# Performance work log

Measured on AMD Instinct MI355X. Metric: run time of the kernel, lower is better.

## Reference

```python
import jax, jax.numpy as jnp
import numpy as np
from jax import lax

B, T, I, H, O = 256, 512, 64, 128, 2  # batch, seq_len, input_size, hidden_size, output_size


def gru_layer(x, Wih, Whh, bih, bhh, reverse):
    # x: [B,T,in_dim], Wih: [3H,in_dim], Whh: [3H,H]; PyTorch gate order: r, z, n
    xw = jnp.einsum('bti,gi->btg', x, Wih) + bih  # precompute input projections [B,T,3H]

    def step(h, xw_t):
        gh = h @ Whh.T + bhh  # [B,3H]
        r = jax.nn.sigmoid(xw_t[:, :H] + gh[:, :H])
        z = jax.nn.sigmoid(xw_t[:, H:2 * H] + gh[:, H:2 * H])
        n = jnp.tanh(xw_t[:, 2 * H:] + r * gh[:, 2 * H:])
        h_new = (1.0 - z) * n + z * h
        return h_new, h_new

    h0 = jnp.zeros((x.shape[0], H), x.dtype)
    _, hs = lax.scan(step, h0, jnp.swapaxes(xw, 0, 1), reverse=reverse)
    # lax.scan with reverse=True stacks outputs aligned to original time order,
    # matching PyTorch's bidirectional GRU output layout.
    return jnp.swapaxes(hs, 0, 1)  # [B,T,H]


def gru_forward(x, params, fc_w, fc_b):
    h = x
    for (Wf, Uf, bf, cf, Wb, Ub, bb, cb) in params:
        fwd = gru_layer(h, Wf, Uf, bf, cf, reverse=False)
        bwd = gru_layer(h, Wb, Ub, bb, cb, reverse=True)
        h = jnp.concatenate([fwd, bwd], axis=-1)  # [B,T,2H]
    last = jax.nn.relu(h[:, -1, :])  # relu then take last timestep (equivalent order)
    return last @ fc_w.T + fc_b  # [B,O]


def setup_inputs() -> dict:
    key = jax.random.key(0)
    ks = iter(jax.random.split(key, 24))
    s = 1.0 / np.sqrt(H)  # PyTorch GRU init scale
    u = lambda shape: jax.random.uniform(next(ks), shape, jnp.float32, -s, s)
    inp = {"x": jax.random.normal(next(ks), (B, T, I), jnp.float32)}
    for l, in_dim in enumerate([I, 2 * H]):
        for d in ("f", "b"):
            inp[f"Wih{l}{d}"] = u((3 * H, in_dim))
            inp[f"Whh{l}{d}"] = u((3 * H, H))
            inp[f"bih{l}{d}"] = u((3 * H,))
            inp[f"bhh{l}{d}"] = u((3 * H,))
    inp["fc_w"] = u((O, 2 * H))
    inp["fc_b"] = u((O,))
    return inp


def reference(x, Wih0f, Whh0f, bih0f, bhh0f, Wih0b, Whh0b, bih0b, bhh0b,
              Wih1f, Whh1f, bih1f, bhh1f, Wih1b, Whh1b, bih1b, bhh1b,
              fc_w, fc_b):
    params = [(Wih0f, Whh0f, bih0f, bhh0f, Wih0b, Whh0b, bih0b, bhh0b),
              (Wih1f, Whh1f, bih1f, bhh1f, Wih1b, Whh1b, bih1b, bhh1b)]
    return gru_forward(x, params, fc_w, fc_b)
```

## Files before the change

kernel.cpp:

```cpp
#include <hip/hip_runtime.h>
#include <hip/hip_fp16.h>

#define B_  256
#define T_  512
#define I_  64
#define H_  128
#define G_  384
#define HC  256

#define O_OUT0 0ull
#define O_XW1  67108864ull
#define O_X16  O_XW1
#define O_WP   167772160ull
#define O_H1F  (O_WP + 196608ull)
#define O_WF16 (O_H1F + 131072ull)

typedef _Float16 h8 __attribute__((ext_vector_type(8)));
typedef _Float16 h2 __attribute__((ext_vector_type(2)));
typedef float    f4 __attribute__((ext_vector_type(4)));

#define MFMA16 __builtin_amdgcn_mfma_f32_16x16x32_f16

__device__ __forceinline__ float sigm(float x)   { return __builtin_amdgcn_rcpf(1.f + __expf(-x)); }
__device__ __forceinline__ float tanh_f(float x) { return 1.f - 2.f * __builtin_amdgcn_rcpf(1.f + __expf(2.f * x)); }

__device__ __forceinline__ void bar_lds() {
    asm volatile("s_waitcnt lgkmcnt(0)\n\ts_barrier" ::: "memory");
}

__device__ __forceinline__ h8 load_w8(const float* src) {
    f4 a = *(const f4*)src;
    f4 b = *(const f4*)(src + 4);
    h8 v;
    v[0]=(_Float16)a[0]; v[1]=(_Float16)a[1]; v[2]=(_Float16)a[2]; v[3]=(_Float16)a[3];
    v[4]=(_Float16)b[0]; v[5]=(_Float16)b[1]; v[6]=(_Float16)b[2]; v[7]=(_Float16)b[3];
    return v;
}

__global__ void prep(const float* __restrict__ x, _Float16* __restrict__ x16,
                     const float* __restrict__ Wf, _Float16* __restrict__ wf16,
                     const float* __restrict__ W1b, __half2* __restrict__ wp) {
    const int bid = blockIdx.x;
    const int tid = threadIdx.x;
    if (bid < 4096) {
        int i = bid * 256 + tid;
        const float* s = x + (size_t)i * 8;
        f4 a = *(const f4*)s, b = *(const f4*)(s + 4);
        h8 v;
        v[0]=(_Float16)a[0]; v[1]=(_Float16)a[1]; v[2]=(_Float16)a[2]; v[3]=(_Float16)a[3];
        v[4]=(_Float16)b[0]; v[5]=(_Float16)b[1]; v[6]=(_Float16)b[2]; v[7]=(_Float16)b[3];
        *(h8*)(x16 + (size_t)i * 8) = v;
    } else if (bid < 4144) {
        int i = (bid - 4096) * 256 + tid;
        const float* s = Wf + (size_t)i * 8;
        f4 a = *(const f4*)s, b = *(const f4*)(s + 4);
        h8 v;
        v[0]=(_Float16)a[0]; v[1]=(_Float16)a[1]; v[2]=(_Float16)a[2]; v[3]=(_Float16)a[3];
        v[4]=(_Float16)b[0]; v[5]=(_Float16)b[1]; v[6]=(_Float16)b[2]; v[7]=(_Float16)b[3];
        *(h8*)(wf16 + (size_t)i * 8) = v;
    } else {
        int i = (bid - 4144) * 256 + tid;
        int c = i % G_;
        int k2 = i / G_;
        wp[i] = __halves2half2(__float2half(W1b[c * 256 + 2 * k2]),
                               __float2half(W1b[c * 256 + 2 * k2 + 1]));
    }
}

__launch_bounds__(512, 1)
__global__ void scan_l0(const _Float16* __restrict__ x16,
                        const float* __restrict__ Wih_f, const float* __restrict__ Whh_f,
                        const float* __restrict__ bih_f, const float* __restrict__ bhh_f,
                        const float* __restrict__ Wih_b, const float* __restrict__ Whh_b,
                        const float* __restrict__ bih_b, const float* __restrict__ bhh_b,
                        _Float16* __restrict__ out0) {
    __shared__ __align__(16) _Float16 s_h[2][16 * 128];

    const int tid  = threadIdx.x;
    const int lane = tid & 63;
    const int w    = tid >> 6;
    const int dir  = blockIdx.y;
    const int b0   = blockIdx.x * 4;

    const float* Wih = dir ? Wih_b : Wih_f;
    const float* Whh = dir ? Whh_b : Whh_f;
    const float* bih = dir ? bih_b : bih_f;
    const float* bhh = dir ? bhh_b : bhh_f;

    for (int i = tid; i < 2 * 16 * 128; i += 512) ((_Float16*)s_h)[i] = (_Float16)0.f;

    const int ln15 = lane & 15;
    const int lq   = lane >> 4;
    const int col  = 16 * w + ln15;

    h8 bh[3][4], bx[3][2];
    float seedR = bih[col] + bhh[col];
    float seedZ = bih[H_ + col] + bhh[H_ + col];
    float bihN  = bih[2 * H_ + col];
    float bhhN  = bhh[2 * H_ + col];
#pragma unroll
    for (int g = 0; g < 3; g++) {
        int n = g * H_ + col;
#pragma unroll
        for (int kt = 0; kt < 4; kt++) bh[g][kt] = load_w8(Whh + (size_t)n * H_ + kt * 32 + lq * 8);
#pragma unroll
        for (int kt = 0; kt < 2; kt++) bx[g][kt] = load_w8(Wih + (size_t)n * I_ + kt * 32 + lq * 8);
    }
    const int arow = ln15 & 12;
    int offh[4];
#pragma unroll
    for (int kt = 0; kt < 4; kt++)
        offh[kt] = arow * 128 + (((kt * 4 + lq) ^ arow) & 15) * 8;
    const int row0  = lq * 4;
    const int offw0 = row0 * 128 + ((((col >> 3) ^ row0) & 15)) * 8 + (col & 7);

    const _Float16* xbase = x16 + ((size_t)(b0 + (ln15 >> 2)) * T_) * I_ + lq * 8;

    const f4 z4 = (f4){0.f, 0.f, 0.f, 0.f};
    const f4 sR4 = (f4){seedR, seedR, seedR, seedR};
    const f4 sZ4 = (f4){seedZ, seedZ, seedZ, seedZ};
    const f4 sXn4 = (f4){bihN, bihN, bihN, bihN};
    const f4 sHn4 = (f4){bhhN, bhhN, bhhN, bhhN};

    _Float16* op = out0 + ((size_t)(b0 + lq) * T_ + (dir ? (T_ - 1) : 0)) * HC + dir * H_ + col;
    const int ostep = dir ? -HC : HC;
    const _Float16* xpA = xbase + (size_t)(dir ? (T_ - 4) : 3) * I_;
    const _Float16* xpB = xbase + (size_t)(dir ? (T_ - 5) : 4) * I_;
    const int xstep = dir ? -(2 * I_) : (2 * I_);

    float hF = 0.f;
    float xr0, xz0, xn0, xr1, xz1, xn1;
    h8 xvA0, xvA1, xvB0, xvB1;
    {
        int t0 = dir ? (T_ - 1) : 0;
        int t1 = dir ? (T_ - 2) : 1;
        int t2 = dir ? (T_ - 3) : 2;
        h8 xc0 = *(const h8*)(xbase + (size_t)t0 * I_);
        h8 xc1 = *(const h8*)(xbase + (size_t)t0 * I_ + 32);
        xvA0 = *(const h8*)(xbase + (size_t)t1 * I_);
        xvA1 = *(const h8*)(xbase + (size_t)t1 * I_ + 32);
        xvB0 = *(const h8*)(xbase + (size_t)t2 * I_);
        xvB1 = *(const h8*)(xbase + (size_t)t2 * I_ + 32);
        f4 aXr = MFMA16(xc1, bx[0][1], MFMA16(xc0, bx[0][0], sR4, 0, 0, 0), 0, 0, 0);
        f4 aXz = MFMA16(xc1, bx[1][1], MFMA16(xc0, bx[1][0], sZ4, 0, 0, 0), 0, 0, 0);
        f4 aXn = MFMA16(xc1, bx[2][1], MFMA16(xc0, bx[2][0], sXn4, 0, 0, 0), 0, 0, 0);
        xr0 = aXr[0]; xz0 = aXz[0]; xn0 = aXn[0];
    }
    __syncthreads();

#pragma unroll 1
    for (int t = 0; t < T_; t += 2) {
        {
            h8 ah0 = *(const h8*)&s_h[0][offh[0]];
            h8 ah1 = *(const h8*)&s_h[0][offh[1]];
            h8 ah2 = *(const h8*)&s_h[0][offh[2]];
            h8 ah3 = *(const h8*)&s_h[0][offh[3]];
            f4 hRa = MFMA16(ah1, bh[0][1], MFMA16(ah0, bh[0][0], z4, 0, 0, 0), 0, 0, 0);
            f4 hRb = MFMA16(ah3, bh[0][3], MFMA16(ah2, bh[0][2], z4, 0, 0, 0), 0, 0, 0);
            f4 hZa = MFMA16(ah1, bh[1][1], MFMA16(ah0, bh[1][0], z4, 0, 0, 0), 0, 0, 0);
            f4 hZb = MFMA16(ah3, bh[1][3], MFMA16(ah2, bh[1][2], z4, 0, 0, 0), 0, 0, 0);
            f4 hNa = MFMA16(ah1, bh[2][1], MFMA16(ah0, bh[2][0], sHn4, 0, 0, 0), 0, 0, 0);
            f4 hNb = MFMA16(ah3, bh[2][3], MFMA16(ah2, bh[2][2], z4, 0, 0, 0), 0, 0, 0);
            float r = sigm(xr0 + hRa[0] + hRb[0]);
            float z = sigm(xz0 + hZa[0] + hZb[0]);
            float n = tanh_f(xn0 + r * (hNa[0] + hNb[0]));
            float h = n + z * (hF - n);
            hF = h;
            s_h[1][offw0] = (_Float16)h;
            *op = (_Float16)h; op += ostep;
            {
                f4 aXr = MFMA16(xvA1, bx[0][1], MFMA16(xvA0, bx[0][0], sR4, 0, 0, 0), 0, 0, 0);
                f4 aXz = MFMA16(xvA1, bx[1][1], MFMA16(xvA0, bx[1][0], sZ4, 0, 0, 0), 0, 0, 0);
                f4 aXn = MFMA16(xvA1, bx[2][1], MFMA16(xvA0, bx[2][0], sXn4, 0, 0, 0), 0, 0, 0);
                xr1 = aXr[0]; xz1 = aXz[0]; xn1 = aXn[0];
            }
            if (t + 3 < T_) {
                xvA0 = *(const h8*)(xpA);
                xvA1 = *(const h8*)(xpA + 32);
                xpA += xstep;
            }
            bar_lds();
        }
        {
            h8 ah0 = *(const h8*)&s_h[1][offh[0]];
            h8 ah1 = *(const h8*)&s_h[1][offh[1]];
            h8 ah2 = *(const h8*)&s_h[1][offh[2]];
            h8 ah3 = *(const h8*)&s_h[1][offh[3]];
            f4 hRa = MFMA16(ah1, bh[0][1], MFMA16(ah0, bh[0][0], z4, 0, 0, 0), 0, 0, 0);
            f4 hRb = MFMA16(ah3, bh[0][3], MFMA16(ah2, bh[0][2], z4, 0, 0, 0), 0, 0, 0);
            f4 hZa = MFMA16(ah1, bh[1][1], MFMA16(ah0, bh[1][0], z4, 0, 0, 0), 0, 0, 0);
            f4 hZb = MFMA16(ah3, bh[1][3], MFMA16(ah2, bh[1][2], z4, 0, 0, 0), 0, 0, 0);
            f4 hNa = MFMA16(ah1, bh[2][1], MFMA16(ah0, bh[2][0], sHn4, 0, 0, 0), 0, 0, 0);
            f4 hNb = MFMA16(ah3, bh[2][3], MFMA16(ah2, bh[2][2], z4, 0, 0, 0), 0, 0, 0);
            float r = sigm(xr1 + hRa[0] + hRb[0]);
            float z = sigm(xz1 + hZa[0] + hZb[0]);
            float n = tanh_f(xn1 + r * (hNa[0] + hNb[0]));
            float h = n + z * (hF - n);
            hF = h;
            s_h[0][offw0] = (_Float16)h;
            *op = (_Float16)h; op += ostep;
            if (t + 2 < T_) {
                f4 aXr = MFMA16(xvB1, bx[0][1], MFMA16(xvB0, bx[0][0], sR4, 0, 0, 0), 0, 0, 0);
                f4 aXz = MFMA16(xvB1, bx[1][1], MFMA16(xvB0, bx[1][0], sZ4, 0, 0, 0), 0, 0, 0);
                f4 aXn = MFMA16(xvB1, bx[2][1], MFMA16(xvB0, bx[2][0], sXn4, 0, 0, 0), 0, 0, 0);
                xr0 = aXr[0]; xz0 = aXz[0]; xn0 = aXn[0];
            }
            if (t + 4 < T_) {
                xvB0 = *(const h8*)(xpB);
                xvB1 = *(const h8*)(xpB + 32);
                xpB += xstep;
            }
            bar_lds();
        }
    }
}

__launch_bounds__(256, 1)
__global__ void gemm_xw1(const _Float16* __restrict__ A,
                         const _Float16* __restrict__ Bw,
                         const float* __restrict__ bias,
                         _Float16* __restrict__ C) {
    __shared__ __align__(16) _Float16 sA[2][64 * 64];
    __shared__ __align__(16) _Float16 sB[2][384 * 64];
    const int tid  = threadIdx.x;
    const int lane = tid & 63;
    const int w    = tid >> 6;
    const int wm   = w & 1, wn = w >> 1;
    const int ln15 = lane & 15, lq = lane >> 4;
    const size_t m0 = (size_t)blockIdx.x * 64;

    f4 acc[2][12] = {};

    int aRow[2], aG[2], aOff[2];
#pragma unroll
    for (int k = 0; k < 2; k++) {
        int idx = k * 256 + tid;
        aRow[k] = idx >> 3; aG[k] = idx & 7;
        aOff[k] = aRow[k] * 64 + ((aG[k] ^ (aRow[k] & 7)) & 7) * 8;
    }
    int bRow[12], bG[12], bOff[12];
#pragma unroll
    for (int k = 0; k < 12; k++) {
        int idx = k * 256 + tid;
        bRow[k] = idx >> 3; bG[k] = idx & 7;
        bOff[k] = bRow[k] * 64 + ((bG[k] ^ (bRow[k] & 7)) & 7) * 8;
    }
    int offA[2][2], offB[12][2];
#pragma unroll
    for (int mt = 0; mt < 2; mt++)
#pragma unroll
        for (int kt = 0; kt < 2; kt++) {
            int row = wm * 32 + mt * 16 + ln15;
            offA[mt][kt] = row * 64 + (((kt * 4 + lq) ^ (row & 7)) & 7) * 8;
        }
#pragma unroll
    for (int nt = 0; nt < 12; nt++)
#pragma unroll
        for (int kt = 0; kt < 2; kt++) {
            int row = wn * 192 + nt * 16 + ln15;
            offB[nt][kt] = row * 64 + (((kt * 4 + lq) ^ (row & 7)) & 7) * 8;
        }

    {
        h8 av[2], bv[12];
#pragma unroll
        for (int k = 0; k < 2; k++) av[k] = *(const h8*)(A + (m0 + aRow[k]) * 256 + aG[k] * 8);
#pragma unroll
        for (int k = 0; k < 12; k++) bv[k] = *(const h8*)(Bw + (size_t)bRow[k] * 256 + bG[k] * 8);
#pragma unroll
        for (int k = 0; k < 2; k++) *(h8*)&sA[0][aOff[k]] = av[k];
#pragma unroll
        for (int k = 0; k < 12; k++) *(h8*)&sB[0][bOff[k]] = bv[k];
        bar_lds();
    }

#pragma unroll
    for (int c = 0; c < 4; c++) {
        const int cur = c & 1;
        h8 av[2], bv[12];
        if (c < 3) {
#pragma unroll
            for (int k = 0; k < 2; k++)
                av[k] = *(const h8*)(A + (m0 + aRow[k]) * 256 + (c + 1) * 64 + aG[k] * 8);
#pragma unroll
            for (int k = 0; k < 12; k++)
                bv[k] = *(const h8*)(Bw + (size_t)bRow[k] * 256 + (c + 1) * 64 + bG[k] * 8);
        }
#pragma unroll
        for (int kt = 0; kt < 2; kt++) {
            h8 af0 = *(const h8*)&sA[cur][offA[0][kt]];
            h8 af1 = *(const h8*)&sA[cur][offA[1][kt]];
#pragma unroll
            for (int nt = 0; nt < 12; nt++) {
                h8 bf = *(const h8*)&sB[cur][offB[nt][kt]];
                acc[0][nt] = MFMA16(af0, bf, acc[0][nt], 0, 0, 0);
                acc[1][nt] = MFMA16(af1, bf, acc[1][nt], 0, 0, 0);
            }
        }
        if (c < 3) {
#pragma unroll
            for (int k = 0; k < 2; k++) *(h8*)&sA[cur ^ 1][aOff[k]] = av[k];
#pragma unroll
            for (int k = 0; k < 12; k++) *(h8*)&sB[cur ^ 1][bOff[k]] = bv[k];
            bar_lds();
        }
    }
#pragma unroll
    for (int nt = 0; nt < 12; nt++) {
        int col = wn * 192 + nt * 16 + ln15;
        float bb = bias[col];
        int pcol = (col < 256) ? ((col & 127) * 2 + (col >> 7)) : col;
#pragma unroll
        for (int mt = 0; mt < 2; mt++) {
            size_t row = m0 + wm * 32 + mt * 16 + lq * 4;
#pragma unroll
            for (int reg = 0; reg < 4; reg++)
                C[(row + reg) * G_ + pcol] = (_Float16)(acc[mt][nt][reg] + bb);
        }
    }
}

__launch_bounds__(512, 1)
__global__ void scan_l1(const _Float16* __restrict__ xw1,
                        const float* __restrict__ Whh,
                        const float* __restrict__ bhh,
                        float* __restrict__ h1f) {
    __shared__ __align__(16) _Float16 s_h[2][16 * 128];

    const int tid  = threadIdx.x;
    const int lane = tid & 63;
    const int w    = tid >> 6;
    const int b0   = blockIdx.x * 4;

    for (int i = tid; i < 2 * 16 * 128; i += 512) ((_Float16*)s_h)[i] = (_Float16)0.f;

    const int ln15 = lane & 15;
    const int lq   = lane >> 4;
    const int col  = 16 * w + ln15;

    h8 bh[3][4];
    float bhhF[3];
#pragma unroll
    for (int g = 0; g < 3; g++) {
        int n = g * H_ + col;
        bhhF[g] = bhh[n];
#pragma unroll
        for (int kt = 0; kt < 4; kt++) bh[g][kt] = load_w8(Whh + (size_t)n * H_ + kt * 32 + lq * 8);
    }
    const int arow = ln15 & 12;
    int offh[4];
#pragma unroll
    for (int kt = 0; kt < 4; kt++)
        offh[kt] = arow * 128 + (((kt * 4 + lq) ^ arow) & 15) * 8;
    const int row0  = lq * 4;
    const int offw0 = row0 * 128 + ((((col >> 3) ^ row0) & 15)) * 8 + (col & 7);

    const _Float16* rzbase = xw1 + ((size_t)(b0 + lq) * T_) * G_ + 2 * col;
    const _Float16* nbase  = xw1 + ((size_t)(b0 + lq) * T_) * G_ + 256 + col;

    const f4 z4 = (f4){0.f, 0.f, 0.f, 0.f};
    const f4 sR4 = (f4){bhhF[0], bhhF[0], bhhF[0], bhhF[0]};
    const f4 sZ4 = (f4){bhhF[1], bhhF[1], bhhF[1], bhhF[1]};
    const f4 sN4 = (f4){bhhF[2], bhhF[2], bhhF[2], bhhF[2]};

    __syncthreads();

    float hF = 0.f;
    h2 rzA = *(const h2*)(rzbase);
    h2 rzB = *(const h2*)(rzbase + G_);
    _Float16 nA = *nbase;
    _Float16 nB = *(nbase + G_);
    const _Float16* rzP2 = rzbase + 2 * G_;
    const _Float16* nP2  = nbase  + 2 * G_;
    const _Float16* rzP3 = rzbase + 3 * G_;
    const _Float16* nP3  = nbase  + 3 * G_;

#pragma unroll 1
    for (int s = 0; s < T_; s += 2) {
        {
            h8 ah0 = *(const h8*)&s_h[0][offh[0]];
            h8 ah1 = *(const h8*)&s_h[0][offh[1]];
            h8 ah2 = *(const h8*)&s_h[0][offh[2]];
            h8 ah3 = *(const h8*)&s_h[0][offh[3]];
            float xr = (float)rzA[0], xz = (float)rzA[1], xn = (float)nA;
            if (s + 2 < T_) {
                rzA = *(const h2*)rzP2;
                nA  = *nP2;
                rzP2 += 2 * G_; nP2 += 2 * G_;
            }
            f4 hRa = MFMA16(ah1, bh[0][1], MFMA16(ah0, bh[0][0], sR4, 0, 0, 0), 0, 0, 0);
            f4 hRb = MFMA16(ah3, bh[0][3], MFMA16(ah2, bh[0][2], z4, 0, 0, 0), 0, 0, 0);
            f4 hZa = MFMA16(ah1, bh[1][1], MFMA16(ah0, bh[1][0], sZ4, 0, 0, 0), 0, 0, 0);
            f4 hZb = MFMA16(ah3, bh[1][3], MFMA16(ah2, bh[1][2], z4, 0, 0, 0), 0, 0, 0);
            f4 hNa = MFMA16(ah1, bh[2][1], MFMA16(ah0, bh[2][0], sN4, 0, 0, 0), 0, 0, 0);
            f4 hNb = MFMA16(ah3, bh[2][3], MFMA16(ah2, bh[2][2], z4, 0, 0, 0), 0, 0, 0);
            float r = sigm(xr + hRa[0] + hRb[0]);
            float z = sigm(xz + hZa[0] + hZb[0]);
            float n = tanh_f(xn + r * (hNa[0] + hNb[0]));
            float h = n + z * (hF - n);
            hF = h;
            s_h[1][offw0] = (_Float16)h;
            bar_lds();
        }
        {
            h8 ah0 = *(const h8*)&s_h[1][offh[0]];
            h8 ah1 = *(const h8*)&s_h[1][offh[1]];
            h8 ah2 = *(const h8*)&s_h[1][offh[2]];
            h8 ah3 = *(const h8*)&s_h[1][offh[3]];
            float xr = (float)rzB[0], xz = (float)rzB[1], xn = (float)nB;
            if (s + 3 < T_) {
                rzB = *(const h2*)rzP3;
                nB  = *nP3;
                rzP3 += 2 * G_; nP3 += 2 * G_;
            }
            f4 hRa = MFMA16(ah1, bh[0][1], MFMA16(ah0, bh[0][0], sR4, 0, 0, 0), 0, 0, 0);
            f4 hRb = MFMA16(ah3, bh[0][3], MFMA16(ah2, bh[0][2], z4, 0, 0, 0), 0, 0, 0);
            f4 hZa = MFMA16(ah1, bh[1][1], MFMA16(ah0, bh[1][0], sZ4, 0, 0, 0), 0, 0, 0);
            f4 hZb = MFMA16(ah3, bh[1][3], MFMA16(ah2, bh[1][2], z4, 0, 0, 0), 0, 0, 0);
            f4 hNa = MFMA16(ah1, bh[2][1], MFMA16(ah0, bh[2][0], sN4, 0, 0, 0), 0, 0, 0);
            f4 hNb = MFMA16(ah3, bh[2][3], MFMA16(ah2, bh[2][2], z4, 0, 0, 0), 0, 0, 0);
            float r = sigm(xr + hRa[0] + hRb[0]);
            float z = sigm(xz + hZa[0] + hZb[0]);
            float n = tanh_f(xn + r * (hNa[0] + hNb[0]));
            float h = n + z * (hF - n);
            hF = h;
            s_h[0][offw0] = (_Float16)h;
            bar_lds();
        }
    }
    h1f[(size_t)(b0 + lq) * H_ + col] = hF;
}

__launch_bounds__(384)
__global__ void final_k(const _Float16* __restrict__ out0,
                        const float* __restrict__ h1f,
                        const __half2* __restrict__ w1b,
                        const float* __restrict__ bih1b, const float* __restrict__ bhh1b,
                        const float* __restrict__ fcw, const float* __restrict__ fcb,
                        float* __restrict__ out) {
    __shared__ __align__(16) float s_x1[HC];
    __shared__ __align__(16) float s_xw[G_];
    __shared__ __align__(16) float s_hc[HC];
    __shared__ float s_red[8];
    const int tid = threadIdx.x;
    const int b = blockIdx.x;
    if (tid < HC)
        s_x1[tid] = (float)out0[((size_t)b * T_ + (T_ - 1)) * HC + tid];
    __syncthreads();
    {
        float acc0 = 0.f, acc1 = 0.f;
        const float2* xv = (const float2*)s_x1;
#pragma unroll 8
        for (int k2 = 0; k2 < 128; k2 += 2) {
            float2 w0 = __half22float2(w1b[k2 * G_ + tid]);
            float2 w1 = __half22float2(w1b[(k2 + 1) * G_ + tid]);
            float2 a0 = xv[k2], a1 = xv[k2 + 1];
            acc0 += a0.x * w0.x + a0.y * w0.y;
            acc1 += a1.x * w1.x + a1.y * w1.y;
        }
        s_xw[tid] = bih1b[tid] + acc0 + acc1;
    }
    __syncthreads();
    if (tid < H_) {
        int j = tid;
        float rg = sigm(s_xw[j] + bhh1b[j]);
        float zg = sigm(s_xw[H_ + j] + bhh1b[H_ + j]);
        float ng = tanh_f(s_xw[2 * H_ + j] + rg * bhh1b[2 * H_ + j]);
        float hb = (1.f - zg) * ng;
        s_hc[H_ + j] = fmaxf(hb, 0.f);
        s_hc[j] = fmaxf(h1f[(size_t)b * H_ + j], 0.f);
    }
    __syncthreads();
    if (tid < HC) {
        float hv = s_hc[tid];
        float p0 = hv * fcw[tid];
        float p1 = hv * fcw[HC + tid];
#pragma unroll
        for (int off = 32; off; off >>= 1) {
            p0 += __shfl_down(p0, off);
            p1 += __shfl_down(p1, off);
        }
        if ((tid & 63) == 0) { s_red[(tid >> 6) * 2] = p0; s_red[(tid >> 6) * 2 + 1] = p1; }
    }
    __syncthreads();
    if (tid == 0) {
        out[b * 2 + 0] = fcb[0] + s_red[0] + s_red[2] + s_red[4] + s_red[6];
        out[b * 2 + 1] = fcb[1] + s_red[1] + s_red[3] + s_red[5] + s_red[7];
    }
}

extern "C" void kernel_launch(void* const* d_in, const int* in_sizes, int n_in,
                              void* d_out, int out_size, void* d_ws, size_t ws_size,
                              hipStream_t stream) {
    (void)in_sizes; (void)n_in; (void)out_size; (void)ws_size;
    const float* x     = (const float*)d_in[0];
    const float* Wih0f = (const float*)d_in[1];
    const float* Whh0f = (const float*)d_in[2];
    const float* bih0f = (const float*)d_in[3];
    const float* bhh0f = (const float*)d_in[4];
    const float* Wih0b = (const float*)d_in[5];
    const float* Whh0b = (const float*)d_in[6];
    const float* bih0b = (const float*)d_in[7];
    const float* bhh0b = (const float*)d_in[8];
    const float* Wih1f = (const float*)d_in[9];
    const float* Whh1f = (const float*)d_in[10];
    const float* bih1f = (const float*)d_in[11];
    const float* bhh1f = (const float*)d_in[12];
    const float* Wih1b = (const float*)d_in[13];
    const float* bih1b = (const float*)d_in[15];
    const float* bhh1b = (const float*)d_in[16];
    const float* fcw   = (const float*)d_in[17];
    const float* fcb   = (const float*)d_in[18];

    char* ws = (char*)d_ws;
    _Float16* out0 = (_Float16*)(ws + O_OUT0);
    _Float16* xw1  = (_Float16*)(ws + O_XW1);
    _Float16* x16  = (_Float16*)(ws + O_X16);
    __half2*  wp   = (__half2*)(ws + O_WP);
    float*    h1f  = (float*)(ws + O_H1F);
    _Float16* wf16 = (_Float16*)(ws + O_WF16);
    float*    out  = (float*)d_out;

    prep<<<4336, 256, 0, stream>>>(x, x16, Wih1f, wf16, Wih1b, wp);

    scan_l0<<<dim3(64, 2), 512, 0, stream>>>(x16, Wih0f, Whh0f, bih0f, bhh0f,
                                             Wih0b, Whh0b, bih0b, bhh0b, out0);

    gemm_xw1<<<2048, 256, 0, stream>>>(out0, wf16, bih1f, xw1);

    scan_l1<<<64, 512, 0, stream>>>(xw1, Whh1f, bhh1f, h1f);

    final_k<<<256, 384, 0, stream>>>(out0, h1f, wp, bih1b, bhh1b, fcw, fcb, out);
}
```

Baseline: 578.8 us.

## Process two independent batch groups per block in GRU scan kernels

Each scan block now handles 8 batch rows as two independent 4-row groups, with separate LDS hidden-state buffers, halving the grid for both layer-0 and layer-1 scans. The two independent MFMA chains are interleaved so that one group's matrix products and activations can hide the latency of the other within each serial timestep. MFMA accumulation is also reordered to interleave gates. In exchange the per-step work per block doubles, register pressure rises, and only 64 or 32 blocks run on the device, leaving most CUs idle.

```diff
diff --git a/kernel.cpp b/kernel.cpp
--- a/kernel.cpp
+++ b/kernel.cpp
@@ -74,20 +74,20 @@
                         const float* __restrict__ Wih_b, const float* __restrict__ Whh_b,
                         const float* __restrict__ bih_b, const float* __restrict__ bhh_b,
                         _Float16* __restrict__ out0) {
-    __shared__ __align__(16) _Float16 s_h[2][16 * 128];
+    __shared__ __align__(16) _Float16 s_h[2][2][16 * 128];
 
     const int tid  = threadIdx.x;
     const int lane = tid & 63;
     const int w    = tid >> 6;
     const int dir  = blockIdx.y;
-    const int b0   = blockIdx.x * 4;
+    const int b0   = blockIdx.x * 8;
 
     const float* Wih = dir ? Wih_b : Wih_f;
     const float* Whh = dir ? Whh_b : Whh_f;
     const float* bih = dir ? bih_b : bih_f;
     const float* bhh = dir ? bhh_b : bhh_f;
 
-    for (int i = tid; i < 2 * 16 * 128; i += 512) ((_Float16*)s_h)[i] = (_Float16)0.f;
+    for (int i = tid; i < 2 * 2 * 16 * 128; i += 512) ((_Float16*)s_h)[i] = (_Float16)0.f;
 
     const int ln15 = lane & 15;
     const int lq   = lane >> 4;
@@ -114,101 +114,147 @@
     const int row0  = lq * 4;
     const int offw0 = row0 * 128 + ((((col >> 3) ^ row0) & 15)) * 8 + (col & 7);
 
-    const _Float16* xbase = x16 + ((size_t)(b0 + (ln15 >> 2)) * T_) * I_ + lq * 8;
-
     const f4 z4 = (f4){0.f, 0.f, 0.f, 0.f};
     const f4 sR4 = (f4){seedR, seedR, seedR, seedR};
     const f4 sZ4 = (f4){seedZ, seedZ, seedZ, seedZ};
     const f4 sXn4 = (f4){bihN, bihN, bihN, bihN};
     const f4 sHn4 = (f4){bhhN, bhhN, bhhN, bhhN};
 
-    _Float16* op = out0 + ((size_t)(b0 + lq) * T_ + (dir ? (T_ - 1) : 0)) * HC + dir * H_ + col;
+    const _Float16* xbase[2];
+    _Float16* op[2];
+    const _Float16* xpA[2];
+    const _Float16* xpB[2];
+#pragma unroll
+    for (int g = 0; g < 2; g++) {
+        int bg = b0 + g * 4;
+        xbase[g] = x16 + ((size_t)(bg + (ln15 >> 2)) * T_) * I_ + lq * 8;
+        op[g] = out0 + ((size_t)(bg + lq) * T_ + (dir ? (T_ - 1) : 0)) * HC + dir * H_ + col;
+        xpA[g] = xbase[g] + (size_t)(dir ? (T_ - 4) : 3) * I_;
+        xpB[g] = xbase[g] + (size_t)(dir ? (T_ - 5) : 4) * I_;
+    }
     const int ostep = dir ? -HC : HC;
-    const _Float16* xpA = xbase + (size_t)(dir ? (T_ - 4) : 3) * I_;
-    const _Float16* xpB = xbase + (size_t)(dir ? (T_ - 5) : 4) * I_;
     const int xstep = dir ? -(2 * I_) : (2 * I_);
 
-    float hF = 0.f;
-    float xr0, xz0, xn0, xr1, xz1, xn1;
-    h8 xvA0, xvA1, xvB0, xvB1;
-    {
+    float hF[2] = {0.f, 0.f};
+    float xr0[2], xz0[2], xn0[2], xr1[2], xz1[2], xn1[2];
+    h8 xvA0[2], xvA1[2], xvB0[2], xvB1[2];
+#pragma unroll
+    for (int g = 0; g < 2; g++) {
         int t0 = dir ? (T_ - 1) : 0;
         int t1 = dir ? (T_ - 2) : 1;
         int t2 = dir ? (T_ - 3) : 2;
-        h8 xc0 = *(const h8*)(xbase + (size_t)t0 * I_);
-        h8 xc1 = *(const h8*)(xbase + (size_t)t0 * I_ + 32);
-        xvA0 = *(const h8*)(xbase + (size_t)t1 * I_);
-        xvA1 = *(const h8*)(xbase + (size_t)t1 * I_ + 32);
-        xvB0 = *(const h8*)(xbase + (size_t)t2 * I_);
-        xvB1 = *(const h8*)(xbase + (size_t)t2 * I_ + 32);
-        f4 aXr = MFMA16(xc1, bx[0][1], MFMA16(xc0, bx[0][0], sR4, 0, 0, 0), 0, 0, 0);
-        f4 aXz = MFMA16(xc1, bx[1][1], MFMA16(xc0, bx[1][0], sZ4, 0, 0, 0), 0, 0, 0);
-        f4 aXn = MFMA16(xc1, bx[2][1], MFMA16(xc0, bx[2][0], sXn4, 0, 0, 0), 0, 0, 0);
-        xr0 = aXr[0]; xz0 = aXz[0]; xn0 = aXn[0];
+        h8 xc0 = *(const h8*)(xbase[g] + (size_t)t0 * I_);
+        h8 xc1 = *(const h8*)(xbase[g] + (size_t)t0 * I_ + 32);
+        xvA0[g] = *(const h8*)(xbase[g] + (size_t)t1 * I_);
+        xvA1[g] = *(const h8*)(xbase[g] + (size_t)t1 * I_ + 32);
+        xvB0[g] = *(const h8*)(xbase[g] + (size_t)t2 * I_);
+        xvB1[g] = *(const h8*)(xbase[g] + (size_t)t2 * I_ + 32);
+        f4 aXr = sR4, aXz = sZ4, aXn = sXn4;
+        aXr = MFMA16(xc0, bx[0][0], aXr, 0, 0, 0);
+        aXz = MFMA16(xc0, bx[1][0], aXz, 0, 0, 0);
+        aXn = MFMA16(xc0, bx[2][0], aXn, 0, 0, 0);
+        aXr = MFMA16(xc1, bx[0][1], aXr, 0, 0, 0);
+        aXz = MFMA16(xc1, bx[1][1], aXz, 0, 0, 0);
+        aXn = MFMA16(xc1, bx[2][1], aXn, 0, 0, 0);
+        xr0[g] = aXr[0]; xz0[g] = aXz[0]; xn0[g] = aXn[0];
     }
     __syncthreads();
 
 #pragma unroll 1
     for (int t = 0; t < T_; t += 2) {
         {
-            h8 ah0 = *(const h8*)&s_h[0][offh[0]];
-            h8 ah1 = *(const h8*)&s_h[0][offh[1]];
-            h8 ah2 = *(const h8*)&s_h[0][offh[2]];
-            h8 ah3 = *(const h8*)&s_h[0][offh[3]];
-            f4 hRa = MFMA16(ah1, bh[0][1], MFMA16(ah0, bh[0][0], z4, 0, 0, 0), 0, 0, 0);
-            f4 hRb = MFMA16(ah3, bh[0][3], MFMA16(ah2, bh[0][2], z4, 0, 0, 0), 0, 0, 0);
-            f4 hZa = MFMA16(ah1, bh[1][1], MFMA16(ah0, bh[1][0], z4, 0, 0, 0), 0, 0, 0);
-            f4 hZb = MFMA16(ah3, bh[1][3], MFMA16(ah2, bh[1][2], z4, 0, 0, 0), 0, 0, 0);
-            f4 hNa = MFMA16(ah1, bh[2][1], MFMA16(ah0, bh[2][0], sHn4, 0, 0, 0), 0, 0, 0);
-            f4 hNb = MFMA16(ah3, bh[2][3], MFMA16(ah2, bh[2][2], z4, 0, 0, 0), 0, 0, 0);
-            float r = sigm(xr0 + hRa[0] + hRb[0]);
-            float z = sigm(xz0 + hZa[0] + hZb[0]);
-            float n = tanh_f(xn0 + r * (hNa[0] + hNb[0]));
-            float h = n + z * (hF - n);
-            hF = h;
-            s_h[1][offw0] = (_Float16)h;
-            *op = (_Float16)h; op += ostep;
-            {
-                f4 aXr = MFMA16(xvA1, bx[0][1], MFMA16(xvA0, bx[0][0], sR4, 0, 0, 0), 0, 0, 0);
-                f4 aXz = MFMA16(xvA1, bx[1][1], MFMA16(xvA0, bx[1][0], sZ4, 0, 0, 0), 0, 0, 0);
-                f4 aXn = MFMA16(xvA1, bx[2][1], MFMA16(xvA0, bx[2][0], sXn4, 0, 0, 0), 0, 0, 0);
-                xr1 = aXr[0]; xz1 = aXz[0]; xn1 = aXn[0];
-            }
-            if (t + 3 < T_) {
-                xvA0 = *(const h8*)(xpA);
-                xvA1 = *(const h8*)(xpA + 32);
-                xpA += xstep;
+            h8 ah[2][4];
+            f4 hRa[2], hRb[2], hZa[2], hZb[2], hNa[2], hNb[2];
+#pragma unroll
+            for (int g = 0; g < 2; g++) {
+#pragma unroll
+                for (int kt = 0; kt < 4; kt++) ah[g][kt] = *(const h8*)&s_h[g][0][offh[kt]];
+                hRa[g] = z4; hRb[g] = z4; hZa[g] = z4; hZb[g] = z4; hNa[g] = sHn4; hNb[g] = z4;
+                hRa[g] = MFMA16(ah[g][0], bh[0][0], hRa[g], 0, 0, 0);
+                hZa[g] = MFMA16(ah[g][0], bh[1][0], hZa[g], 0, 0, 0);
+                hNa[g] = MFMA16(ah[g][0], bh[2][0], hNa[g], 0, 0, 0);
+                hRb[g] = MFMA16(ah[g][2], bh[0][2], hRb[g], 0, 0, 0);
+                hZb[g] = MFMA16(ah[g][2], bh[1][2], hZb[g], 0, 0, 0);
+                hNb[g] = MFMA16(ah[g][2], bh[2][2], hNb[g], 0, 0, 0);
+                hRa[g] = MFMA16(ah[g][1], bh[0][1], hRa[g], 0, 0, 0);
+                hZa[g] = MFMA16(ah[g][1], bh[1][1], hZa[g], 0, 0, 0);
+                hNa[g] = MFMA16(ah[g][1], bh[2][1], hNa[g], 0, 0, 0);
+                hRb[g] = MFMA16(ah[g][3], bh[0][3], hRb[g], 0, 0, 0);
+                hZb[g] = MFMA16(ah[g][3], bh[1][3], hZb[g], 0, 0, 0);
+                hNb[g] = MFMA16(ah[g][3], bh[2][3], hNb[g], 0, 0, 0);
+            }
+#pragma unroll
+            for (int g = 0; g < 2; g++) {
+                float r = sigm(xr0[g] + hRa[g][0] + hRb[g][0]);
+                float z = sigm(xz0[g] + hZa[g][0] + hZb[g][0]);
+                float n = tanh_f(xn0[g] + r * (hNa[g][0] + hNb[g][0]));
+                float h = n + z * (hF[g] - n);
+                hF[g] = h;
+                s_h[g][1][offw0] = (_Float16)h;
+                *op[g] = (_Float16)h; op[g] += ostep;
+                {
+                    f4 aXr = sR4, aXz = sZ4, aXn = sXn4;
+                    aXr = MFMA16(xvA0[g], bx[0][0], aXr, 0, 0, 0);
+                    aXz = MFMA16(xvA0[g], bx[1][0], aXz, 0, 0, 0);
+                    aXn = MFMA16(xvA0[g], bx[2][0], aXn, 0, 0, 0);
+                    aXr = MFMA16(xvA1[g], bx[0][1], aXr, 0, 0, 0);
+                    aXz = MFMA16(xvA1[g], bx[1][1], aXz, 0, 0, 0);
+                    aXn = MFMA16(xvA1[g], bx[2][1], aXn, 0, 0, 0);
+                    xr1[g] = aXr[0]; xz1[g] = aXz[0]; xn1[g] = aXn[0];
+                }
+                if (t + 3 < T_) {
+                    xvA0[g] = *(const h8*)(xpA[g]);
+                    xvA1[g] = *(const h8*)(xpA[g] + 32);
+                    xpA[g] += xstep;
+                }
             }
             bar_lds();
         }
         {
-            h8 ah0 = *(const h8*)&s_h[1][offh[0]];
-            h8 ah1 = *(const h8*)&s_h[1][offh[1]];
-            h8 ah2 = *(const h8*)&s_h[1][offh[2]];
-            h8 ah3 = *(const h8*)&s_h[1][offh[3]];
-            f4 hRa = MFMA16(ah1, bh[0][1], MFMA16(ah0, bh[0][0], z4, 0, 0, 0), 0, 0, 0);
-            f4 hRb = MFMA16(ah3, bh[0][3], MFMA16(ah2, bh[0][2], z4, 0, 0, 0), 0, 0, 0);
-            f4 hZa = MFMA16(ah1, bh[1][1], MFMA16(ah0, bh[1][0], z4, 0, 0, 0), 0, 0, 0);
-            f4 hZb = MFMA16(ah3, bh[1][3], MFMA16(ah2, bh[1][2], z4, 0, 0, 0), 0, 0, 0);
-            f4 hNa = MFMA16(ah1, bh[2][1], MFMA16(ah0, bh[2][0], sHn4, 0, 0, 0), 0, 0, 0);
-            f4 hNb = MFMA16(ah3, bh[2][3], MFMA16(ah2, bh[2][2], z4, 0, 0, 0), 0, 0, 0);
-            float r = sigm(xr1 + hRa[0] + hRb[0]);
-            float z = sigm(xz1 + hZa[0] + hZb[0]);
-            float n = tanh_f(xn1 + r * (hNa[0] + hNb[0]));
-            float h = n + z * (hF - n);
-            hF = h;
-            s_h[0][offw0] = (_Float16)h;
-            *op = (_Float16)h; op += ostep;
-            if (t + 2 < T_) {
-                f4 aXr = MFMA16(xvB1, bx[0][1], MFMA16(xvB0, bx[0][0], sR4, 0, 0, 0), 0, 0, 0);
-                f4 aXz = MFMA16(xvB1, bx[1][1], MFMA16(xvB0, bx[1][0], sZ4, 0, 0, 0), 0, 0, 0);
-                f4 aXn = MFMA16(xvB1, bx[2][1], MFMA16(xvB0, bx[2][0], sXn4, 0, 0, 0), 0, 0, 0);
-                xr0 = aXr[0]; xz0 = aXz[0]; xn0 = aXn[0];
-            }
-            if (t + 4 < T_) {
-                xvB0 = *(const h8*)(xpB);
-                xvB1 = *(const h8*)(xpB + 32);
-                xpB += xstep;
+            h8 ah[2][4];
+            f4 hRa[2], hRb[2], hZa[2], hZb[2], hNa[2], hNb[2];
+#pragma unroll
+            for (int g = 0; g < 2; g++) {
+#pragma unroll
+                for (int kt = 0; kt < 4; kt++) ah[g][kt] = *(const h8*)&s_h[g][1][offh[kt]];
+                hRa[g] = z4; hRb[g] = z4; hZa[g] = z4; hZb[g] = z4; hNa[g] = sHn4; hNb[g] = z4;
+                hRa[g] = MFMA16(ah[g][0], bh[0][0], hRa[g], 0, 0, 0);
+                hZa[g] = MFMA16(ah[g][0], bh[1][0], hZa[g], 0, 0, 0);
+                hNa[g] = MFMA16(ah[g][0], bh[2][0], hNa[g], 0, 0, 0);
+                hRb[g] = MFMA16(ah[g][2], bh[0][2], hRb[g], 0, 0, 0);
+                hZb[g] = MFMA16(ah[g][2], bh[1][2], hZb[g], 0, 0, 0);
+                hNb[g] = MFMA16(ah[g][2], bh[2][2], hNb[g], 0, 0, 0);
+                hRa[g] = MFMA16(ah[g][1], bh[0][1], hRa[g], 0, 0, 0);
+                hZa[g] = MFMA16(ah[g][1], bh[1][1], hZa[g], 0, 0, 0);
+                hNa[g] = MFMA16(ah[g][1], bh[2][1], hNa[g], 0, 0, 0);
+                hRb[g] = MFMA16(ah[g][3], bh[0][3], hRb[g], 0, 0, 0);
+                hZb[g] = MFMA16(ah[g][3], bh[1][3], hZb[g], 0, 0, 0);
+                hNb[g] = MFMA16(ah[g][3], bh[2][3], hNb[g], 0, 0, 0);
+            }
+#pragma unroll
+            for (int g = 0; g < 2; g++) {
+                float r = sigm(xr1[g] + hRa[g][0] + hRb[g][0]);
+                float z = sigm(xz1[g] + hZa[g][0] + hZb[g][0]);
+                float n = tanh_f(xn1[g] + r * (hNa[g][0] + hNb[g][0]));
+                float h = n + z * (hF[g] - n);
+                hF[g] = h;
+                s_h[g][0][offw0] = (_Float16)h;
+                *op[g] = (_Float16)h; op[g] += ostep;
+                if (t + 2 < T_) {
+                    f4 aXr = sR4, aXz = sZ4, aXn = sXn4;
+                    aXr = MFMA16(xvB0[g], bx[0][0], aXr, 0, 0, 0);
+                    aXz = MFMA16(xvB0[g], bx[1][0], aXz, 0, 0, 0);
+                    aXn = MFMA16(xvB0[g], bx[2][0], aXn, 0, 0, 0);
+                    aXr = MFMA16(xvB1[g], bx[0][1], aXr, 0, 0, 0);
+                    aXz = MFMA16(xvB1[g], bx[1][1], aXz, 0, 0, 0);
+                    aXn = MFMA16(xvB1[g], bx[2][1], aXn, 0, 0, 0);
+                    xr0[g] = aXr[0]; xz0[g] = aXz[0]; xn0[g] = aXn[0];
+                }
+                if (t + 4 < T_) {
+                    xvB0[g] = *(const h8*)(xpB[g]);
+                    xvB1[g] = *(const h8*)(xpB[g] + 32);
+                    xpB[g] += xstep;
+                }
             }
             bar_lds();
         }
@@ -325,14 +371,14 @@
                         const float* __restrict__ Whh,
                         const float* __restrict__ bhh,
                         float* __restrict__ h1f) {
-    __shared__ __align__(16) _Float16 s_h[2][16 * 128];
+    __shared__ __align__(16) _Float16 s_h[2][2][16 * 128];
 
     const int tid  = threadIdx.x;
     const int lane = tid & 63;
     const int w    = tid >> 6;
-    const int b0   = blockIdx.x * 4;
-
-    for (int i = tid; i < 2 * 16 * 128; i += 512) ((_Float16*)s_h)[i] = (_Float16)0.f;
+    const int b0   = blockIdx.x * 8;
+
+    for (int i = tid; i < 2 * 2 * 16 * 128; i += 512) ((_Float16*)s_h)[i] = (_Float16)0.f;
 
     const int ln15 = lane & 15;
     const int lq   = lane >> 4;
@@ -355,80 +401,125 @@
     const int row0  = lq * 4;
     const int offw0 = row0 * 128 + ((((col >> 3) ^ row0) & 15)) * 8 + (col & 7);
 
-    const _Float16* rzbase = xw1 + ((size_t)(b0 + lq) * T_) * G_ + 2 * col;
-    const _Float16* nbase  = xw1 + ((size_t)(b0 + lq) * T_) * G_ + 256 + col;
-
     const f4 z4 = (f4){0.f, 0.f, 0.f, 0.f};
     const f4 sR4 = (f4){bhhF[0], bhhF[0], bhhF[0], bhhF[0]};
     const f4 sZ4 = (f4){bhhF[1], bhhF[1], bhhF[1], bhhF[1]};
     const f4 sN4 = (f4){bhhF[2], bhhF[2], bhhF[2], bhhF[2]};
 
+    const _Float16* rzbase[2];
+    const _Float16* nbase[2];
+#pragma unroll
+    for (int g = 0; g < 2; g++) {
+        int bg = b0 + g * 4;
+        rzbase[g] = xw1 + ((size_t)(bg + lq) * T_) * G_ + 2 * col;
+        nbase[g]  = xw1 + ((size_t)(bg + lq) * T_) * G_ + 256 + col;
+    }
+
     __syncthreads();
 
-    float hF = 0.f;
-    h2 rzA = *(const h2*)(rzbase);
-    h2 rzB = *(const h2*)(rzbase + G_);
-    _Float16 nA = *nbase;
-    _Float16 nB = *(nbase + G_);
-    const _Float16* rzP2 = rzbase + 2 * G_;
-    const _Float16* nP2  = nbase  + 2 * G_;
-    const _Float16* rzP3 = rzbase + 3 * G_;
-    const _Float16* nP3  = nbase  + 3 * G_;
+    float hF[2] = {0.f, 0.f};
+    h2 rzA[2], rzB[2];
+    _Float16 nA[2], nB[2];
+    const _Float16* rzP2[2];
+    const _Float16* nP2[2];
+    const _Float16* rzP3[2];
+    const _Float16* nP3[2];
+#pragma unroll
+    for (int g = 0; g < 2; g++) {
+        rzA[g] = *(const h2*)(rzbase[g]);
+        rzB[g] = *(const h2*)(rzbase[g] + G_);
+        nA[g] = *nbase[g];
+        nB[g] = *(nbase[g] + G_);
+        rzP2[g] = rzbase[g] + 2 * G_;
+        nP2[g]  = nbase[g]  + 2 * G_;
+        rzP3[g] = rzbase[g] + 3 * G_;
+        nP3[g]  = nbase[g]  + 3 * G_;
+    }
 
 #pragma unroll 1
     for (int s = 0; s < T_; s += 2) {
         {
-            h8 ah0 = *(const h8*)&s_h[0][offh[0]];
-            h8 ah1 = *(const h8*)&s_h[0][offh[1]];
-            h8 ah2 = *(const h8*)&s_h[0][offh[2]];
-            h8 ah3 = *(const h8*)&s_h[0][offh[3]];
-            float xr = (float)rzA[0], xz = (float)rzA[1], xn = (float)nA;
-            if (s + 2 < T_) {
-                rzA = *(const h2*)rzP2;
-                nA  = *nP2;
-                rzP2 += 2 * G_; nP2 += 2 * G_;
-            }
-            f4 hRa = MFMA16(ah1, bh[0][1], MFMA16(ah0, bh[0][0], sR4, 0, 0, 0), 0, 0, 0);
-            f4 hRb = MFMA16(ah3, bh[0][3], MFMA16(ah2, bh[0][2], z4, 0, 0, 0), 0, 0, 0);
-            f4 hZa = MFMA16(ah1, bh[1][1], MFMA16(ah0, bh[1][0], sZ4, 0, 0, 0), 0, 0, 0);
-            f4 hZb = MFMA16(ah3, bh[1][3], MFMA16(ah2, bh[1][2], z4, 0, 0, 0), 0, 0, 0);
-            f4 hNa = MFMA16(ah1, bh[2][1], MFMA16(ah0, bh[2][0], sN4, 0, 0, 0), 0, 0, 0);
-            f4 hNb = MFMA16(ah3, bh[2][3], MFMA16(ah2, bh[2][2], z4, 0, 0, 0), 0, 0, 0);
-            float r = sigm(xr + hRa[0] + hRb[0]);
-            float z = sigm(xz + hZa[0] + hZb[0]);
-            float n = tanh_f(xn + r * (hNa[0] + hNb[0]));
-            float h = n + z * (hF - n);
-            hF = h;
-            s_h[1][offw0] = (_Float16)h;
+            h8 ah[2][4];
+            f4 hRa[2], hRb[2], hZa[2], hZb[2], hNa[2], hNb[2];
+            float xr[2], xz[2], xn[2];
+#pragma unroll
+            for (int g = 0; g < 2; g++) {
+#pragma unroll
+                for (int kt = 0; kt < 4; kt++) ah[g][kt] = *(const h8*)&s_h[g][0][offh[kt]];
+                xr[g] = (float)rzA[g][0]; xz[g] = (float)rzA[g][1]; xn[g] = (float)nA[g];
+                if (s + 2 < T_) {
+                    rzA[g] = *(const h2*)rzP2[g];
+                    nA[g]  = *nP2[g];
+                    rzP2[g] += 2 * G_; nP2[g] += 2 * G_;
+                }
+                hRa[g] = sR4; hRb[g] = z4; hZa[g] = sZ4; hZb[g] = z4; hNa[g] = sN4; hNb[g] = z4;
+                hRa[g] = MFMA16(ah[g][0], bh[0][0], hRa[g], 0, 0, 0);
+                hZa[g] = MFMA16(ah[g][0], bh[1][0], hZa[g], 0, 0, 0);
+                hNa[g] = MFMA16(ah[g][0], bh[2][0], hNa[g], 0, 0, 0);
+                hRb[g] = MFMA16(ah[g][2], bh[0][2], hRb[g], 0, 0, 0);
+                hZb[g] = MFMA16(ah[g][2], bh[1][2], hZb[g], 0, 0, 0);
+                hNb[g] = MFMA16(ah[g][2], bh[2][2], hNb[g], 0, 0, 0);
+                hRa[g] = MFMA16(ah[g][1], bh[0][1], hRa[g], 0, 0, 0);
+                hZa[g] = MFMA16(ah[g][1], bh[1][1], hZa[g], 0, 0, 0);
+                hNa[g] = MFMA16(ah[g][1], bh[2][1], hNa[g], 0, 0, 0);
+                hRb[g] = MFMA16(ah[g][3], bh[0][3], hRb[g], 0, 0, 0);
+                hZb[g] = MFMA16(ah[g][3], bh[1][3], hZb[g], 0, 0, 0);
+                hNb[g] = MFMA16(ah[g][3], bh[2][3], hNb[g], 0, 0, 0);
+            }
+#pragma unroll
+            for (int g = 0; g < 2; g++) {
+                float r = sigm(xr[g] + hRa[g][0] + hRb[g][0]);
+                float z = sigm(xz[g] + hZa[g][0] + hZb[g][0]);
+                float n = tanh_f(xn[g] + r * (hNa[g][0] + hNb[g][0]));
+                float h = n + z * (hF[g] - n);
+                hF[g] = h;
+                s_h[g][1][offw0] = (_Float16)h;
+            }
             bar_lds();
         }
         {
-            h8 ah0 = *(const h8*)&s_h[1][offh[0]];
-            h8 ah1 = *(const h8*)&s_h[1][offh[1]];
-            h8 ah2 = *(const h8*)&s_h[1][offh[2]];
-            h8 ah3 = *(const h8*)&s_h[1][offh[3]];
-            float xr = (float)rzB[0], xz = (float)rzB[1], xn = (float)nB;
-            if (s + 3 < T_) {
-                rzB = *(const h2*)rzP3;
-                nB  = *nP3;
-                rzP3 += 2 * G_; nP3 += 2 * G_;
-            }
-            f4 hRa = MFMA16(ah1, bh[0][1], MFMA16(ah0, bh[0][0], sR4, 0, 0, 0), 0, 0, 0);
-            f4 hRb = MFMA16(ah3, bh[0][3], MFMA16(ah2, bh[0][2], z4, 0, 0, 0), 0, 0, 0);
-            f4 hZa = MFMA16(ah1, bh[1][1], MFMA16(ah0, bh[1][0], sZ4, 0, 0, 0), 0, 0, 0);
-            f4 hZb = MFMA16(ah3, bh[1][3], MFMA16(ah2, bh[1][2], z4, 0, 0, 0), 0, 0, 0);
-            f4 hNa = MFMA16(ah1, bh[2][1], MFMA16(ah0, bh[2][0], sN4, 0, 0, 0), 0, 0, 0);
-            f4 hNb = MFMA16(ah3, bh[2][3], MFMA16(ah2, bh[2][2], z4, 0, 0, 0), 0, 0, 0);
-            float r = sigm(xr + hRa[0] + hRb[0]);
-            float z = sigm(xz + hZa[0] + hZb[0]);
-            float n = tanh_f(xn + r * (hNa[0] + hNb[0]));
-            float h = n + z * (hF - n);
-            hF = h;
-            s_h[0][offw0] = (_Float16)h;
+            h8 ah[2][4];
+            f4 hRa[2], hRb[2], hZa[2], hZb[2], hNa[2], hNb[2];
+            float xr[2], xz[2], xn[2];
+#pragma unroll
+            for (int g = 0; g < 2; g++) {
+#pragma unroll
+                for (int kt = 0; kt < 4; kt++) ah[g][kt] = *(const h8*)&s_h[g][1][offh[kt]];
+                xr[g] = (float)rzB[g][0]; xz[g] = (float)rzB[g][1]; xn[g] = (float)nB[g];
+                if (s + 3 < T_) {
+                    rzB[g] = *(const h2*)rzP3[g];
+                    nB[g]  = *nP3[g];
+                    rzP3[g] += 2 * G_; nP3[g] += 2 * G_;
+                }
+                hRa[g] = sR4; hRb[g] = z4; hZa[g] = sZ4; hZb[g] = z4; hNa[g] = sN4; hNb[g] = z4;
+                hRa[g] = MFMA16(ah[g][0], bh[0][0], hRa[g], 0, 0, 0);
+                hZa[g] = MFMA16(ah[g][0], bh[1][0], hZa[g], 0, 0, 0);
+                hNa[g] = MFMA16(ah[g][0], bh[2][0], hNa[g], 0, 0, 0);
+                hRb[g] = MFMA16(ah[g][2], bh[0][2], hRb[g], 0, 0, 0);
+                hZb[g] = MFMA16(ah[g][2], bh[1][2], hZb[g], 0, 0, 0);
+                hNb[g] = MFMA16(ah[g][2], bh[2][2], hNb[g], 0, 0, 0);
+                hRa[g] = MFMA16(ah[g][1], bh[0][1], hRa[g], 0, 0, 0);
+                hZa[g] = MFMA16(ah[g][1], bh[1][1], hZa[g], 0, 0, 0);
+                hNa[g] = MFMA16(ah[g][1], bh[2][1], hNa[g], 0, 0, 0);
+                hRb[g] = MFMA16(ah[g][3], bh[0][3], hRb[g], 0, 0, 0);
+                hZb[g] = MFMA16(ah[g][3], bh[1][3], hZb[g], 0, 0, 0);
+                hNb[g] = MFMA16(ah[g][3], bh[2][3], hNb[g], 0, 0, 0);
+            }
+#pragma unroll
+            for (int g = 0; g < 2; g++) {
+                float r = sigm(xr[g] + hRa[g][0] + hRb[g][0]);
+                float z = sigm(xz[g] + hZa[g][0] + hZb[g][0]);
+                float n = tanh_f(xn[g] + r * (hNa[g][0] + hNb[g][0]));
+                float h = n + z * (hF[g] - n);
+                hF[g] = h;
+                s_h[g][0][offw0] = (_Float16)h;
+            }
             bar_lds();
         }
     }
-    h1f[(size_t)(b0 + lq) * H_ + col] = hF;
+#pragma unroll
+    for (int g = 0; g < 2; g++)
+        h1f[(size_t)(b0 + g * 4 + lq) * H_ + col] = hF[g];
 }
 
 __launch_bounds__(384)
@@ -523,12 +614,12 @@
 
     prep<<<4336, 256, 0, stream>>>(x, x16, Wih1f, wf16, Wih1b, wp);
 
-    scan_l0<<<dim3(64, 2), 512, 0, stream>>>(x16, Wih0f, Whh0f, bih0f, bhh0f,
+    scan_l0<<<dim3(32, 2), 512, 0, stream>>>(x16, Wih0f, Whh0f, bih0f, bhh0f,
                                              Wih0b, Whh0b, bih0b, bhh0b, out0);
 
     gemm_xw1<<<2048, 256, 0, stream>>>(out0, wf16, bih1f, xw1);
 
-    scan_l1<<<64, 512, 0, stream>>>(xw1, Whh1f, bhh1f, h1f);
+    scan_l1<<<32, 512, 0, stream>>>(xw1, Whh1f, bhh1f, h1f);
 
     final_k<<<256, 384, 0, stream>>>(out0, h1f, wp, bih1b, bhh1b, fcw, fcb, out);
 }
```

New measurement: 894.1 us. 54.5% more time.
